# Kernel optimization log

Measured on AMD Instinct MI355X. Metric: run time of the kernel, lower is better.

The kernel has to match this reference:

```python
import jax, jax.numpy as jnp
import numpy as np

NUM_INPUTS = 256
NUM_OUTPUTS = 256
BATCH = 1024


def build_lhs(ni: int, no: int) -> jnp.ndarray:
    """Constraint matrix of the bipartite flow graph.

    Edge ordering follows the torch code: for output o, for input j -> column o*ni + j.
    Rows 0..ni-1: flow conservation at each input node (sum of outgoing flows = x_i).
    Rows ni..ni+no-1: equality constraints flow(e1) - flow(e2) = 0 for the
    per-output equal_edges pair chosen by in_idx = round(o*ni/no).
    """
    E = ni * no
    lhs = np.zeros((ni + no, E), dtype=np.float32)
    for i in range(ni):
        lhs[i, np.arange(no) * ni + i] = 1.0
    for o in range(no):
        in_idx = round(o * ni / no)
        a = in_idx % ni
        b = (in_idx + 1) % ni
        lhs[ni + o, o * ni + a] += 1.0
        lhs[ni + o, o * ni + b] -= 1.0
    return jnp.asarray(lhs)


def setup_inputs() -> dict:
    key = jax.random.key(0)
    k1, k2 = jax.random.split(key)
    xs = jax.random.normal(k1, (BATCH, NUM_INPUTS), dtype=jnp.float32)
    param = jax.random.normal(k2, (NUM_INPUTS * NUM_OUTPUTS,), dtype=jnp.float32)
    lhs = build_lhs(NUM_INPUTS, NUM_OUTPUTS)
    return {"xs": xs, "param": param, "lhs": lhs}


def reference(xs, param, lhs):
    """Batched constrained flow solve.

    Per sample: f* = argmin ||f - c||^2 s.t. lhs @ f = rhs, with
    c = softplus(param) (edge capacities) and rhs = [x; 0].
    Closed form via KKT: f* = c + lhs^T (lhs lhs^T)^{-1} (rhs - lhs c).
    Outputs are the total inflow at each output node. The torch module solves
    this per sample in a Python loop; here it is vectorized over the batch.
    """
    B = xs.shape[0]
    ni = NUM_INPUTS
    no = NUM_OUTPUTS
    c = jax.nn.softplus(param)                                      # [E]
    rhs = jnp.concatenate([xs, jnp.zeros((B, no), xs.dtype)], 1)    # [B, C]
    M = lhs @ lhs.T                                                 # [C, C] small gram
    d = rhs - (lhs @ c)[None, :]                                    # [B, C]
    lam = jnp.linalg.solve(M, d.T).T                                # [B, C] multipliers
    flow = c[None, :] + lam @ lhs                                   # [B, E]
    # edges grouped by output: column o*ni + j -> output o gets sum over j
    return flow.reshape(B, no, ni).sum(-1)                          # [B, no]
```

## Files before the change

### kernel.cpp

```cpp
#include <hip/hip_runtime.h>
#include <math.h>

#define NI 256
#define NO 256
#define BATCH 1024


__device__ __forceinline__ float softplus_f(float x) {
    return fmaxf(x, 0.0f) + log1pf(expf(-fabsf(x)));
}

__device__ __forceinline__ float wave_reduce_64(float v) {
    #pragma unroll
    for (int off = 32; off > 0; off >>= 1)
        v += __shfl_down(v, off, 64);
    return v;
}

__global__ __launch_bounds__(256) void reduce_kernel(const float* __restrict__ xs,
                                                     const float* __restrict__ param,
                                                     float* __restrict__ ws) {
    const int lane = threadIdx.x & 63;
    const int row = blockIdx.x * 4 + (threadIdx.x >> 6);
    float s;
    if (row < NO) {
        const float4 p = ((const float4*)(param + row * NI))[lane];
        s = softplus_f(p.x) + softplus_f(p.y) + softplus_f(p.z) + softplus_f(p.w);
    } else {
        const float4 x = ((const float4*)(xs + (row - NO) * NI))[lane];
        s = (x.x + x.y) + (x.z + x.w);
    }
    s = wave_reduce_64(s);
    if (lane == 0) ws[row] = s;
}

__global__ __launch_bounds__(256) void out_kernel(const float* __restrict__ ws,
                                                  float* __restrict__ out) {
    __shared__ float lds[4];
    const int o = threadIdx.x;
    const float Co = ws[o];

    float t = wave_reduce_64(Co);
    const int lane = o & 63;
    const int wave = o >> 6;
    if (lane == 0) lds[wave] = t;
    __syncthreads();
    const float total = lds[0] + lds[1] + lds[2] + lds[3];

    const int b0 = blockIdx.x * 4;
    #pragma unroll
    for (int r = 0; r < 4; ++r) {
        const float Sx = ws[NO + b0 + r];
        out[(b0 + r) * NO + o] = Co + (Sx - total) * (1.0f / (float)NO);
    }
}

extern "C" void kernel_launch(void* const* d_in, const int* in_sizes, int n_in,
                              void* d_out, int out_size, void* d_ws, size_t ws_size,
                              hipStream_t stream) {
    const float* xs    = (const float*)d_in[0];
    const float* param = (const float*)d_in[1];
    float* out = (float*)d_out;
    float* ws  = (float*)d_ws;

    reduce_kernel<<<(NO + BATCH) / 4, 256, 0, stream>>>(xs, param, ws);
    out_kernel<<<BATCH / 4, 256, 0, stream>>>(ws, out);
}
```

Measured before the change: 165.0 us.

## Fuse reduction and output kernels into one launch with redundant param softplus

Merges the two kernels into a single kernel of 64 blocks by 1024 threads. Each block recomputes the full softplus row sums of param into LDS, reduces its own 16 xs rows, then writes its output rows. This removes the second launch and the global workspace round trip. The cost is that every block redundantly computes softplus over all 64K params, and only 64 blocks run.

```diff
diff --git a/kernel.cpp b/kernel.cpp
--- a/kernel.cpp
+++ b/kernel.cpp
@@ -5,6 +5,11 @@
 #define NO 256
 #define BATCH 1024
 
+
+#define NBLK 64
+#define RPB (BATCH / NBLK)
+#define NT 1024
+#define NW (NT / 64)
 
 __device__ __forceinline__ float softplus_f(float x) {
     return fmaxf(x, 0.0f) + log1pf(expf(-fabsf(x)));
@@ -17,41 +22,46 @@
     return v;
 }
 
-__global__ __launch_bounds__(256) void reduce_kernel(const float* __restrict__ xs,
-                                                     const float* __restrict__ param,
-                                                     float* __restrict__ ws) {
+__global__ __launch_bounds__(NT) void fused_kernel(const float* __restrict__ xs,
+                                                   const float* __restrict__ param,
+                                                   float* __restrict__ out) {
+    __shared__ float ldsC[NO];
+    __shared__ float ldsS[RPB];
+    __shared__ float ldsT[NW];
+
     const int lane = threadIdx.x & 63;
-    const int row = blockIdx.x * 4 + (threadIdx.x >> 6);
-    float s;
-    if (row < NO) {
-        const float4 p = ((const float4*)(param + row * NI))[lane];
-        s = softplus_f(p.x) + softplus_f(p.y) + softplus_f(p.z) + softplus_f(p.w);
-    } else {
-        const float4 x = ((const float4*)(xs + (row - NO) * NI))[lane];
-        s = (x.x + x.y) + (x.z + x.w);
+    const int wave = threadIdx.x >> 6;
+    const int b0 = blockIdx.x * RPB;
+
+    {
+        const float4 x = ((const float4*)(xs + (size_t)(b0 + wave) * NI))[lane];
+        float s = (x.x + x.y) + (x.z + x.w);
+        s = wave_reduce_64(s);
+        if (lane == 0) ldsS[wave] = s;
     }
-    s = wave_reduce_64(s);
-    if (lane == 0) ws[row] = s;
-}
 
-__global__ __launch_bounds__(256) void out_kernel(const float* __restrict__ ws,
-                                                  float* __restrict__ out) {
-    __shared__ float lds[4];
-    const int o = threadIdx.x;
-    const float Co = ws[o];
+    float tpart = 0.0f;
+    #pragma unroll 4
+    for (int r = 0; r < NO / NW; ++r) {
+        const int row = wave * (NO / NW) + r;
+        const float4 p = ((const float4*)(param + (size_t)row * NI))[lane];
+        float s = softplus_f(p.x) + softplus_f(p.y) + softplus_f(p.z) + softplus_f(p.w);
+        s = wave_reduce_64(s);
+        if (lane == 0) { ldsC[row] = s; tpart += s; }
+    }
+    if (lane == 0) ldsT[wave] = tpart;
+    __syncthreads();
 
-    float t = wave_reduce_64(Co);
-    const int lane = o & 63;
-    const int wave = o >> 6;
-    if (lane == 0) lds[wave] = t;
-    __syncthreads();
-    const float total = lds[0] + lds[1] + lds[2] + lds[3];
+    float total = 0.0f;
+    #pragma unroll
+    for (int w = 0; w < NW; ++w) total += ldsT[w];
 
-    const int b0 = blockIdx.x * 4;
     #pragma unroll
-    for (int r = 0; r < 4; ++r) {
-        const float Sx = ws[NO + b0 + r];
-        out[(b0 + r) * NO + o] = Co + (Sx - total) * (1.0f / (float)NO);
+    for (int i = 0; i < (RPB * NO) / NT; ++i) {
+        const int idx = i * NT + (int)threadIdx.x;
+        const int r = idx >> 8;
+        const int o = idx & 255;
+        out[(size_t)(b0 + r) * NO + o] = ldsC[o] + (ldsS[r] - total) * (1.0f / (float)NO);
     }
 }
 
@@ -61,8 +71,7 @@
     const float* xs    = (const float*)d_in[0];
     const float* param = (const float*)d_in[1];
     float* out = (float*)d_out;
-    float* ws  = (float*)d_ws;
+    (void)d_ws; (void)ws_size;
 
-    reduce_kernel<<<(NO + BATCH) / 4, 256, 0, stream>>>(xs, param, ws);
-    out_kernel<<<BATCH / 4, 256, 0, stream>>>(ws, out);
+    fused_kernel<<<NBLK, NT, 0, stream>>>(xs, param, out);
 }
```

Result: slower. 210.5 us (+27.5%).
